# Kernel optimization log

Hardware: AMD Instinct MI355X
Metric: run time of the kernel (lower is better)

Reference implementation:

```python
import jax, jax.numpy as jnp
import numpy as np

C = 1.0
SQC = C ** 0.5
EPS = 1e-15

def _artanh(x):
    return jnp.arctanh(jnp.clip(x, -1 + 1e-5, 1 - 1e-5))

def _norm(x):
    return jnp.sqrt(jnp.maximum(jnp.sum(x * x, -1, keepdims=True), EPS))

def expmap0(u):
    un = _norm(u)
    return jnp.tanh(SQC * un) * u / (SQC * un)

def logmap0(x):
    xn = _norm(x)
    return _artanh(SQC * xn) * x / (SQC * xn)

def project(x):
    maxnorm = (1.0 - 1e-3) / SQC
    xn = _norm(x)
    return jnp.where(xn > maxnorm, x / xn * maxnorm, x)

def mobius_add(x, y):
    x2 = jnp.sum(x * x, -1, keepdims=True)
    y2 = jnp.sum(y * y, -1, keepdims=True)
    xy = jnp.sum(x * y, -1, keepdims=True)
    num = (1 + 2 * C * xy + C * y2) * x + (1 - C * x2) * y
    den = 1 + 2 * C * xy + C * C * x2 * y2
    return num / jnp.maximum(den, EPS)

def mobius_matvec(M, x):
    xn = _norm(x)
    Mx = x @ M.T
    Mxn = _norm(Mx)
    res = jnp.tanh(Mxn / xn * _artanh(SQC * xn)) * Mx / (Mxn * SQC)
    return jnp.where(Mxn <= 1e-7, jnp.zeros_like(res), res)

def mobius_pointwise_mul(w, x):
    xn = _norm(x)
    wx = w * x
    wxn = _norm(wx)
    res = jnp.tanh(wxn / xn * _artanh(SQC * xn)) * wx / (wxn * SQC)
    return jnp.where(wxn <= 1e-7, jnp.zeros_like(res), res)

def mobius_scalar_mul(r, x):
    # r: [B,1] scalars, x: [P] point -> [B,P]
    xn = _norm(x)
    return jnp.tanh(r * _artanh(SQC * xn)) * x / (xn * SQC)

def poincare_dist(x, y):
    return 2.0 / SQC * _artanh(SQC * _norm(mobius_add(-x, y)))

def dist2plane(x, p, a):
    # x: [B,P], p,a: [K,P] -> [B,K]
    diff = mobius_add(-p[None, :, :], x[:, None, :])  # [B,K,P]
    diff2 = jnp.sum(diff * diff, -1)
    sc_da = jnp.sum(diff * a[None, :, :], -1)
    a_norm = jnp.sqrt(jnp.maximum(jnp.sum(a * a, -1), EPS))  # [K]
    num = 2 * SQC * sc_da
    den = jnp.maximum((1 - C * diff2) * a_norm[None, :], EPS)
    return jnp.arcsinh(num / den) / SQC

def one_rnn_transform(W, h, U, x, b):
    Wh = mobius_matvec(W, h)
    Ux = mobius_matvec(U, x)
    return mobius_add(mobius_add(Wh, Ux), b)

def mobius_gru(x_seq, w_ih, w_hh, b, h0):
    # x_seq: [S,B,E]; w_ih: [3,H,E]; w_hh: [3,H,H]; b: [3,H]
    W_ir, W_ih_, W_iz = w_ih[0], w_ih[1], w_ih[2]
    W_hr, W_hh_, W_hz = w_hh[0], w_hh[1], w_hh[2]
    b_r, b_h, b_z = b[0], b[1], b[2]

    def cell(h, x):
        z = jax.nn.sigmoid(logmap0(one_rnn_transform(W_hz, h, W_iz, x, b_z)))
        r = jax.nn.sigmoid(logmap0(one_rnn_transform(W_hr, h, W_ir, x, b_r)))
        rh = mobius_pointwise_mul(r, h)
        h_tilde = one_rnn_transform(W_hh_, rh, W_ih_, x, b_h)
        delta = mobius_add(-h, h_tilde)
        h_new = mobius_add(h, mobius_pointwise_mul(z, delta))
        return h_new, None

    h_final, _ = jax.lax.scan(cell, h0, x_seq)
    return h_final

def mobius_linear(x, W, b):
    return project(mobius_add(mobius_matvec(W, x), b))


def setup_inputs() -> dict:
    key = jax.random.key(0)
    ks = jax.random.split(key, 20)
    V, E, H, P, K, B, S = 32000, 256, 512, 256, 2, 512, 100
    inp = {
        "embedding": jax.random.normal(ks[0], (V, E), jnp.float32) * 0.1,
        "w_ih_src": jax.random.normal(ks[1], (3, H, E), jnp.float32) * 0.05,
        "w_hh_src": jax.random.normal(ks[2], (3, H, H), jnp.float32) * 0.05,
        "b_src": jax.random.normal(ks[3], (3, H), jnp.float32) * 0.01,
        "w_ih_tgt": jax.random.normal(ks[4], (3, H, E), jnp.float32) * 0.05,
        "w_hh_tgt": jax.random.normal(ks[5], (3, H, H), jnp.float32) * 0.05,
        "b_tgt": jax.random.normal(ks[6], (3, H), jnp.float32) * 0.01,
        "wp_src": jax.random.normal(ks[7], (P, H), jnp.float32) * 0.05,
        "bp_src": jax.random.normal(ks[8], (P,), jnp.float32) * 0.01,
        "wp_tgt": jax.random.normal(ks[9], (P, H), jnp.float32) * 0.05,
        "bp_tgt": jax.random.normal(ks[10], (P,), jnp.float32) * 0.01,
        "dist_bias": jax.random.normal(ks[11], (P,), jnp.float32) * 0.01,
        "plane_p": jax.random.normal(ks[12], (K, P), jnp.float32) * 0.01,
        "plane_a": jax.random.normal(ks[13], (K, P), jnp.float32) * 0.1,
        "source_tokens": jax.random.randint(ks[14], (B, S), 0, V, jnp.int32),
        "target_tokens": jax.random.randint(ks[15], (B, S), 0, V, jnp.int32),
        "alignment": jax.random.randint(ks[16], (B,), 0, B, jnp.int32),
    }
    return inp


def reference(embedding, w_ih_src, w_hh_src, b_src, w_ih_tgt, w_hh_tgt, b_tgt,
              wp_src, bp_src, wp_tgt, bp_tgt, dist_bias, plane_p, plane_a,
              source_tokens, target_tokens, alignment):
    B, S = source_tokens.shape
    H = w_hh_src.shape[-1]
    # euclidean embeddings lifted to the Poincare ball (embedding_type='eucl', hyp cell)
    src = expmap0(embedding[source_tokens]).transpose(1, 0, 2)  # [S,B,E]
    tgt = expmap0(embedding[target_tokens]).transpose(1, 0, 2)
    h0 = jnp.zeros((B, H), src.dtype)
    h_src = mobius_gru(src, w_ih_src, w_hh_src, b_src, h0)
    h_tgt = mobius_gru(tgt, w_ih_tgt, w_hh_tgt, b_tgt, h0)
    h_tgt = h_tgt[alignment]
    src_proj = mobius_linear(h_src, wp_src, bp_src)
    tgt_proj = mobius_linear(h_tgt, wp_tgt, bp_tgt)
    projected = mobius_add(src_proj, tgt_proj)
    d2 = poincare_dist(h_src, h_tgt) ** 2  # [B,1]
    bias = mobius_scalar_mul(d2, dist_bias)  # [B,P]
    projected = mobius_add(projected, bias)
    logits = dist2plane(projected, plane_p, plane_a)  # [B,K]
    return logits
```

## Files before the change

kernel.cpp:

```cpp
#include <hip/hip_runtime.h>
#include <hip/hip_bf16.h>

#define EPSF 1e-15f

__device__ __forceinline__ float artanh_c(float x) {
  x = fminf(fmaxf(x, -1.f + 1e-5f), 1.f - 1e-5f);
  return 0.5f * log1pf(2.f * x / (1.f - x));
}
__device__ __forceinline__ float sigmoidf(float x) {
  return 1.f / (1.f + expf(-x));
}

template<int N>
__device__ __forceinline__ void block_reduce(float* v) {
  __shared__ float s[4][N];
  __syncthreads();
  const int lane = threadIdx.x & 63;
  const int wv = threadIdx.x >> 6;
#pragma unroll
  for (int n = 0; n < N; n++) {
    float x = v[n];
#pragma unroll
    for (int o = 32; o > 0; o >>= 1) x += __shfl_down(x, o);
    if (lane == 0) s[wv][n] = x;
  }
  __syncthreads();
#pragma unroll
  for (int n = 0; n < N; n++) v[n] = s[0][n] + s[1][n] + s[2][n] + s[3][n];
}

__global__ __launch_bounds__(256) void k_tok(
    const float* __restrict__ emb, const int* __restrict__ src_t,
    const int* __restrict__ tgt_t, float4* __restrict__ tokf)
{
  const int item = blockIdx.x * 4 + (threadIdx.x >> 6);
  const int lane = threadIdx.x & 63;
  const int g = item / 51200;
  const int rem = item - g * 51200;
  const int b = rem / 100, s = rem - b * 100;
  const int tok = (g ? tgt_t : src_t)[b * 100 + s];
  const float4 v = ((const float4*)(emb + (size_t)tok * 256))[lane];
  float ss = v.x*v.x + v.y*v.y + v.z*v.z + v.w*v.w;
#pragma unroll
  for (int o = 32; o > 0; o >>= 1) ss += __shfl_xor(ss, o);
  if (lane == 0) {
    const float un = sqrtf(fmaxf(ss, EPSF));
    const float fac = tanhf(un) / un;
    const float xn = sqrtf(fmaxf(fac * fac * ss, EPSF));
    const float axn = artanh_c(xn);
    tokf[item] = make_float4(fac, xn, axn, un);
  }
}

__global__ __launch_bounds__(256) void kx0(
    const float* __restrict__ emb, const int* __restrict__ src_t,
    const int* __restrict__ tgt_t, const float4* __restrict__ tokf,
    float* __restrict__ xb)
{
  const int row = blockIdx.x;
  const int t = threadIdx.x;
  const int g = row >> 9, b = row & 511;
  const int tok = (g ? tgt_t : src_t)[b * 100];
  const float fac = tokf[(g * 512 + b) * 100].x;
  xb[(size_t)row * 256 + t] = fac * emb[(size_t)tok * 256 + t];
}

__global__ __launch_bounds__(256) void gemm_k(
    int mode,
    const float* __restrict__ hbuf, const float* __restrict__ xbuf,
    const float* __restrict__ rhbuf,
    const float* __restrict__ w_ih_src, const float* __restrict__ w_hh_src,
    const float* __restrict__ w_ih_tgt, const float* __restrict__ w_hh_tgt,
    const float* __restrict__ wp_src, const float* __restrict__ wp_tgt,
    const int* __restrict__ alignment,
    float* __restrict__ out)
{
  const int rt = blockIdx.x, ct = blockIdx.y;
  const int rowBase = rt * 64;
  const int tid = threadIdx.x;
  int kdim, ldo, colBase;
  const float* W;
  const float* Abase;
  int gather = 0;
  if (mode == 0) {
    const int chunk = ct >> 3;
    colBase = ct * 64; ldo = 2560;
    const int g = rowBase >> 9;
    const float* wih = g ? w_ih_tgt : w_ih_src;
    const float* whh = g ? w_hh_tgt : w_hh_src;
    if (chunk == 0)      { W = whh + 2 * 512 * 512; Abase = hbuf; kdim = 512; }
    else if (chunk == 1) { W = whh;                 Abase = hbuf; kdim = 512; }
    else {
      kdim = 256; Abase = xbuf;
      W = (chunk == 2) ? (wih + 2 * 512 * 256) : ((chunk == 3) ? wih : (wih + 512 * 256));
    }
    W += (size_t)((ct & 7) * 64) * kdim;
  } else if (mode == 1) {
    const int g = rowBase >> 9;
    W = (g ? w_hh_tgt : w_hh_src) + 512 * 512 + (size_t)(ct * 64) * 512;
    Abase = rhbuf; kdim = 512; ldo = 512; colBase = ct * 64;
  } else {
    const int chunk = ct >> 2;
    colBase = ct * 64; ldo = 512; kdim = 512;
    W = (chunk ? wp_tgt : wp_src) + (size_t)((ct & 3) * 64) * 512;
    Abase = hbuf;
    gather = chunk;
  }
  const int ar = tid >> 2, ak = (tid & 3) * 4;
  int arow = rowBase + ar;
  if (mode == 2 && gather) arow = 512 + alignment[arow];
  const float* Arow = Abase + (size_t)arow * kdim;
  const float* Wrow = W + (size_t)(tid >> 2) * kdim + (tid & 3) * 4;

  __shared__ __align__(16) float As[16][68];
  __shared__ __align__(16) float Bs[16][68];
  float acc[4][4] = {{0.f}};
  const int ty = tid >> 4, tx = tid & 15;

  for (int k0 = 0; k0 < kdim; k0 += 16) {
    const float4 av = *(const float4*)(Arow + k0 + ak);
    const float4 bv = *(const float4*)(Wrow + k0);
    const int bj = tid >> 2;
    As[ak + 0][ar] = av.x; As[ak + 1][ar] = av.y; As[ak + 2][ar] = av.z; As[ak + 3][ar] = av.w;
    Bs[ak + 0][bj] = bv.x; Bs[ak + 1][bj] = bv.y; Bs[ak + 2][bj] = bv.z; Bs[ak + 3][bj] = bv.w;
    __syncthreads();
#pragma unroll
    for (int kk = 0; kk < 16; kk++) {
      const float4 a4 = *(const float4*)(&As[kk][ty * 4]);
      const float4 b4 = *(const float4*)(&Bs[kk][tx * 4]);
      acc[0][0] += a4.x * b4.x; acc[0][1] += a4.x * b4.y; acc[0][2] += a4.x * b4.z; acc[0][3] += a4.x * b4.w;
      acc[1][0] += a4.y * b4.x; acc[1][1] += a4.y * b4.y; acc[1][2] += a4.y * b4.z; acc[1][3] += a4.y * b4.w;
      acc[2][0] += a4.z * b4.x; acc[2][1] += a4.z * b4.y; acc[2][2] += a4.z * b4.z; acc[2][3] += a4.z * b4.w;
      acc[3][0] += a4.w * b4.x; acc[3][1] += a4.w * b4.y; acc[3][2] += a4.w * b4.z; acc[3][3] += a4.w * b4.w;
    }
    __syncthreads();
  }
#pragma unroll
  for (int r = 0; r < 4; r++) {
    float4 o; o.x = acc[r][0]; o.y = acc[r][1]; o.z = acc[r][2]; o.w = acc[r][3];
    *(float4*)(out + (size_t)(rowBase + ty * 4 + r) * ldo + colBase + tx * 4) = o;
  }
}

__global__ __launch_bounds__(256) void k2_gates(
    const float* __restrict__ g1, const float* __restrict__ hb,
    const float* __restrict__ b_src, const float* __restrict__ b_tgt,
    const float4* __restrict__ tokf,
    float* __restrict__ zb, float* __restrict__ rhb,
    float* __restrict__ uhxb, float* __restrict__ rn, int s)
{
  const int row = blockIdx.x;
  const int g = row >> 9, b = row & 511;
  const int t = threadIdx.x;
  const float* bb = g ? b_tgt : b_src;
  const float4 tf = tokf[(g * 512 + b) * 100 + s];
  const float xn_x = tf.y, axn_x = tf.z;
  const float* grow = g1 + (size_t)row * 2560;
  const float* hrow = hb + (size_t)row * 512;

  float h[2], whz[2], whr[2], uxz[2], uxr[2], uxh[2], bz[2], br[2];
  float r6[6] = {0, 0, 0, 0, 0, 0};
#pragma unroll
  for (int e = 0; e < 2; e++) {
    const int j = t + e * 256;
    h[e] = hrow[j];
    whz[e] = grow[j];        whr[e] = grow[512 + j];
    uxz[e] = grow[1024 + j]; uxr[e] = grow[1536 + j];
    uxh[e] = grow[2048 + j];
    bz[e] = bb[1024 + j];    br[e] = bb[j];
    r6[0] += h[e] * h[e];     r6[1] += whz[e] * whz[e]; r6[2] += whr[e] * whr[e];
    r6[3] += uxz[e] * uxz[e]; r6[4] += uxr[e] * uxr[e]; r6[5] += uxh[e] * uxh[e];
  }
  block_reduce<6>(r6);
  const float sh2 = r6[0];
  const float xn_h = sqrtf(fmaxf(sh2, EPSF)), axn_h = artanh_c(xn_h);

  const float mz = sqrtf(fmaxf(r6[1], EPSF)); const float tz = tanhf(mz / xn_h * axn_h);
  const float sz = (mz <= 1e-7f) ? 0.f : tz / mz; const float x2z = (mz <= 1e-7f) ? 0.f : tz * tz;
  const float mr = sqrtf(fmaxf(r6[2], EPSF)); const float tr = tanhf(mr / xn_h * axn_h);
  const float sr = (mr <= 1e-7f) ? 0.f : tr / mr; const float x2r = (mr <= 1e-7f) ? 0.f : tr * tr;
  const float muz = sqrtf(fmaxf(r6[3], EPSF)); const float tuz = tanhf(muz / xn_x * axn_x);
  const float suz = (muz <= 1e-7f) ? 0.f : tuz / muz; const float y2z = (muz <= 1e-7f) ? 0.f : tuz * tuz;
  const float mur = sqrtf(fmaxf(r6[4], EPSF)); const float tur = tanhf(mur / xn_x * axn_x);
  const float sur = (mur <= 1e-7f) ? 0.f : tur / mur; const float y2r = (mur <= 1e-7f) ? 0.f : tur * tur;
  const float muh = sqrtf(fmaxf(r6[5], EPSF)); const float tuh = tanhf(muh / xn_x * axn_x);
  const float suh = (muh <= 1e-7f) ? 0.f : tuh / muh; const float y2u = (muh <= 1e-7f) ? 0.f : tuh * tuh;

  float Wz[2], Uz[2], Wr[2], Ur[2];
  float dd[2] = {0, 0};
#pragma unroll
  for (int e = 0; e < 2; e++) {
    Wz[e] = sz * whz[e]; Uz[e] = suz * uxz[e];
    Wr[e] = sr * whr[e]; Ur[e] = sur * uxr[e];
    dd[0] += Wz[e] * Uz[e]; dd[1] += Wr[e] * Ur[e];
  }
  block_reduce<2>(dd);
  float t1z[2], t1r[2];
  {
    const float xy = dd[0];
    const float iv = 1.f / fmaxf(1.f + 2.f * xy + x2z * y2z, EPSF);
    const float c1 = 1.f + 2.f * xy + y2z, c2 = 1.f - x2z;
#pragma unroll
    for (int e = 0; e < 2; e++) t1z[e] = (c1 * Wz[e] + c2 * Uz[e]) * iv;
  }
  {
    const float xy = dd[1];
    const float iv = 1.f / fmaxf(1.f + 2.f * xy + x2r * y2r, EPSF);
    const float c1 = 1.f + 2.f * xy + y2r, c2 = 1.f - x2r;
#pragma unroll
    for (int e = 0; e < 2; e++) t1r[e] = (c1 * Wr[e] + c2 * Ur[e]) * iv;
  }
  float r6b[6] = {0, 0, 0, 0, 0, 0};
#pragma unroll
  for (int e = 0; e < 2; e++) {
    r6b[0] += t1z[e] * t1z[e]; r6b[1] += t1z[e] * bz[e]; r6b[2] += bz[e] * bz[e];
    r6b[3] += t1r[e] * t1r[e]; r6b[4] += t1r[e] * br[e]; r6b[5] += br[e] * br[e];
  }
  block_reduce<6>(r6b);
  float t2z[2], t2r[2];
  {
    const float x2 = r6b[0], xy = r6b[1], y2 = r6b[2];
    const float iv = 1.f / fmaxf(1.f + 2.f * xy + x2 * y2, EPSF);
    const float c1 = 1.f + 2.f * xy + y2, c2 = 1.f - x2;
#pragma unroll
    for (int e = 0; e < 2; e++) t2z[e] = (c1 * t1z[e] + c2 * bz[e]) * iv;
  }
  {
    const float x2 = r6b[3], xy = r6b[4], y2 = r6b[5];
    const float iv = 1.f / fmaxf(1.f + 2.f * xy + x2 * y2, EPSF);
    const float c1 = 1.f + 2.f * xy + y2, c2 = 1.f - x2;
#pragma unroll
    for (int e = 0; e < 2; e++) t2r[e] = (c1 * t1r[e] + c2 * br[e]) * iv;
  }
  float nn[2] = {0, 0};
#pragma unroll
  for (int e = 0; e < 2; e++) { nn[0] += t2z[e] * t2z[e]; nn[1] += t2r[e] * t2r[e]; }
  block_reduce<2>(nn);
  const float nz = sqrtf(fmaxf(nn[0], EPSF)); const float fz = artanh_c(nz) / nz;
  const float nr = sqrtf(fmaxf(nn[1], EPSF)); const float fr = artanh_c(nr) / nr;
  float zz[2], wx[2];
  float rw[1] = {0};
#pragma unroll
  for (int e = 0; e < 2; e++) {
    zz[e] = sigmoidf(fz * t2z[e]);
    const float rr = sigmoidf(fr * t2r[e]);
    wx[e] = rr * h[e];
    rw[0] += wx[e] * wx[e];
  }
  block_reduce<1>(rw);
  const float wxn = sqrtf(fmaxf(rw[0], EPSF));
  const float trh = tanhf(wxn / xn_h * axn_h);
  const float srh = (wxn <= 1e-7f) ? 0.f : trh / wxn;
  const float xn_rh = (wxn <= 1e-7f) ? sqrtf(EPSF) : fmaxf(trh, sqrtf(EPSF));
  const float axn_rh = artanh_c(xn_rh);
#pragma unroll
  for (int e = 0; e < 2; e++) {
    const int j = t + e * 256;
    zb[(size_t)row * 512 + j] = zz[e];
    rhb[(size_t)row * 512 + j] = srh * wx[e];
    uhxb[(size_t)row * 512 + j] = suh * uxh[e];
  }
  if (t == 0) {
    float* r8 = rn + row * 8;
    r8[0] = xn_h; r8[1] = axn_h; r8[2] = xn_rh; r8[3] = axn_rh; r8[4] = y2u; r8[5] = sh2;
  }
}

__global__ __launch_bounds__(256) void k4_update(
    const float* __restrict__ htm, const float* __restrict__ uhxb,
    const float* __restrict__ zb, float* __restrict__ hb,
    const float* __restrict__ b_src, const float* __restrict__ b_tgt,
    const float* __restrict__ rn, const float4* __restrict__ tokf,
    const int* __restrict__ src_t, const int* __restrict__ tgt_t,
    const float* __restrict__ emb, float* __restrict__ xb, int s)
{
  const int row = blockIdx.x;
  const int g = row >> 9, b = row & 511;
  const int t = threadIdx.x;
  const float* bb = g ? b_tgt : b_src;
  const float* r8 = rn + row * 8;
  const float xn_rh = r8[2], axn_rh = r8[3], y2u = r8[4], sh2 = r8[5];

  float mt_[2], ux[2], z[2], h[2], bh[2];
  float rA[2] = {0, 0};
#pragma unroll
  for (int e = 0; e < 2; e++) {
    const int j = t + e * 256;
    mt_[e] = htm[(size_t)row * 512 + j];
    ux[e] = uhxb[(size_t)row * 512 + j];
    z[e] = zb[(size_t)row * 512 + j];
    h[e] = hb[(size_t)row * 512 + j];
    bh[e] = bb[512 + j];
    rA[0] += mt_[e] * mt_[e];
    rA[1] += mt_[e] * ux[e];
  }
  block_reduce<2>(rA);
  const float m = sqrtf(fmaxf(rA[0], EPSF));
  const float tt = tanhf(m / xn_rh * axn_rh);
  const float st = (m <= 1e-7f) ? 0.f : tt / m;
  const float x2 = (m <= 1e-7f) ? 0.f : tt * tt;
  float t1[2];
  {
    const float xy = st * rA[1];
    const float iv = 1.f / fmaxf(1.f + 2.f * xy + x2 * y2u, EPSF);
    const float c1 = 1.f + 2.f * xy + y2u, c2 = 1.f - x2;
#pragma unroll
    for (int e = 0; e < 2; e++) t1[e] = (c1 * (st * mt_[e]) + c2 * ux[e]) * iv;
  }
  float rB[3] = {0, 0, 0};
#pragma unroll
  for (int e = 0; e < 2; e++) {
    rB[0] += t1[e] * t1[e]; rB[1] += t1[e] * bh[e]; rB[2] += bh[e] * bh[e];
  }
  block_reduce<3>(rB);
  float ht[2];
  {
    const float x2b = rB[0], xy = rB[1], y2 = rB[2];
    const float iv = 1.f / fmaxf(1.f + 2.f * xy + x2b * y2, EPSF);
    const float c1 = 1.f + 2.f * xy + y2, c2 = 1.f - x2b;
#pragma unroll
    for (int e = 0; e < 2; e++) ht[e] = (c1 * t1[e] + c2 * bh[e]) * iv;
  }
  float rC[2] = {0, 0};
#pragma unroll
  for (int e = 0; e < 2; e++) { rC[0] += ht[e] * ht[e]; rC[1] += h[e] * ht[e]; }
  block_reduce<2>(rC);
  float delta[2];
  {
    const float y2 = rC[0], xy = -rC[1];
    const float iv = 1.f / fmaxf(1.f + 2.f * xy + sh2 * y2, EPSF);
    const float c1 = 1.f + 2.f * xy + y2, c2 = 1.f - sh2;
#pragma unroll
    for (int e = 0; e < 2; e++) delta[e] = (c1 * (-h[e]) + c2 * ht[e]) * iv;
  }
  float rD[3] = {0, 0, 0};
#pragma unroll
  for (int e = 0; e < 2; e++) {
    const float w = z[e] * delta[e];
    rD[0] += delta[e] * delta[e];
    rD[1] += w * w;
    rD[2] += h[e] * w;
  }
  block_reduce<3>(rD);
  const float dn = sqrtf(fmaxf(rD[0], EPSF));
  const float axnd = artanh_c(dn);
  const float wxn = sqrtf(fmaxf(rD[1], EPSF));
  const float tzd = tanhf(wxn / dn * axnd);
  const float szd = (wxn <= 1e-7f) ? 0.f : tzd / wxn;
  const float y2zd = (wxn <= 1e-7f) ? 0.f : tzd * tzd;
  {
    const float xy = szd * rD[2];
    const float iv = 1.f / fmaxf(1.f + 2.f * xy + sh2 * y2zd, EPSF);
    const float c1 = 1.f + 2.f * xy + y2zd, c2 = 1.f - sh2;
#pragma unroll
    for (int e = 0; e < 2; e++) {
      const int j = t + e * 256;
      hb[(size_t)row * 512 + j] = (c1 * h[e] + c2 * (szd * z[e] * delta[e])) * iv;
    }
  }
  if (s + 1 < 100) {
    const int tok = (g ? tgt_t : src_t)[b * 100 + s + 1];
    const float fac = tokf[(g * 512 + b) * 100 + s + 1].x;
    xb[(size_t)row * 256 + t] = fac * emb[(size_t)tok * 256 + t];
  }
}

__global__ __launch_bounds__(256) void k_head(
    const float* __restrict__ hb, const float* __restrict__ mxb,
    const float* __restrict__ bp_src, const float* __restrict__ bp_tgt,
    const float* __restrict__ dist_bias, const float* __restrict__ plane_p,
    const float* __restrict__ plane_a, const int* __restrict__ alignment,
    float* __restrict__ outp)
{
  const int b = blockIdx.x;
  const int t = threadIdx.x;
  const int arow = 512 + alignment[b];
  float hs[2], htg[2];
  hs[0] = hb[(size_t)b * 512 + t];      hs[1] = hb[(size_t)b * 512 + 256 + t];
  htg[0] = hb[(size_t)arow * 512 + t];  htg[1] = hb[(size_t)arow * 512 + 256 + t];
  const float mxs = mxb[(size_t)b * 512 + t];
  const float mxt = mxb[(size_t)b * 512 + 256 + t];
  const float bps = bp_src[t], bpt = bp_tgt[t], db = dist_bias[t];
  const float pp0 = plane_p[t], pp1 = plane_p[256 + t];
  const float pa0 = plane_a[t], pa1 = plane_a[256 + t];

  float rA[5] = {0, 0, 0, 0, 0};
#pragma unroll
  for (int e = 0; e < 2; e++) {
    rA[0] += hs[e] * hs[e]; rA[1] += htg[e] * htg[e]; rA[2] += hs[e] * htg[e];
  }
  rA[3] = mxs * mxs; rA[4] = mxt * mxt;
  block_reduce<5>(rA);
  const float shs = rA[0], sht = rA[1], dot_st = rA[2];
  const float xns = sqrtf(fmaxf(shs, EPSF)), axns = artanh_c(xns);
  const float xnt = sqrtf(fmaxf(sht, EPSF)), axnt = artanh_c(xnt);
  const float ms = sqrtf(fmaxf(rA[3], EPSF)); const float ts = tanhf(ms / xns * axns);
  const float ss = (ms <= 1e-7f) ? 0.f : ts / ms; const float x2s = (ms <= 1e-7f) ? 0.f : ts * ts;
  const float mt = sqrtf(fmaxf(rA[4], EPSF)); const float tt = tanhf(mt / xnt * axnt);
  const float st = (mt <= 1e-7f) ? 0.f : tt / mt; const float x2t = (mt <= 1e-7f) ? 0.f : tt * tt;
  const float vs = ss * mxs, vt = st * mxt;

  float rB[5] = {bps * bps, vs * bps, bpt * bpt, vt * bpt, db * db};
  block_reduce<5>(rB);
  float ps, pt;
  {
    const float y2 = rB[0], xy = rB[1];
    const float iv = 1.f / fmaxf(1.f + 2.f * xy + x2s * y2, EPSF);
    ps = ((1.f + 2.f * xy + y2) * vs + (1.f - x2s) * bps) * iv;
  }
  {
    const float y2 = rB[2], xy = rB[3];
    const float iv = 1.f / fmaxf(1.f + 2.f * xy + x2t * y2, EPSF);
    pt = ((1.f + 2.f * xy + y2) * vt + (1.f - x2t) * bpt) * iv;
  }
  float rC[2] = {ps * ps, pt * pt};
  block_reduce<2>(rC);
  {
    const float n = sqrtf(fmaxf(rC[0], EPSF));
    if (n > 0.999f) ps *= 0.999f / n;
  }
  {
    const float n = sqrtf(fmaxf(rC[1], EPSF));
    if (n > 0.999f) pt *= 0.999f / n;
  }
  float df[2];
  {
    const float xy = -dot_st;
    const float iv = 1.f / fmaxf(1.f + 2.f * xy + shs * sht, EPSF);
    const float c1 = 1.f + 2.f * xy + sht, c2 = 1.f - shs;
#pragma unroll
    for (int e = 0; e < 2; e++) df[e] = (c1 * (-hs[e]) + c2 * htg[e]) * iv;
  }
  float rD[4] = {ps * ps, pt * pt, ps * pt, df[0] * df[0] + df[1] * df[1]};
  block_reduce<4>(rD);
  float pr;
  {
    const float x2 = rD[0], y2 = rD[1], xy = rD[2];
    const float iv = 1.f / fmaxf(1.f + 2.f * xy + x2 * y2, EPSF);
    pr = ((1.f + 2.f * xy + y2) * ps + (1.f - x2) * pt) * iv;
  }
  const float dn = sqrtf(fmaxf(rD[3], EPSF));
  const float dist = 2.f * artanh_c(dn);
  const float d2v = dist * dist;
  const float dbn = sqrtf(fmaxf(rB[4], EPSF));
  const float biasv = tanhf(d2v * artanh_c(dbn)) * db / dbn;

  float rE[3] = {pr * pr, biasv * biasv, pr * biasv};
  block_reduce<3>(rE);
  float pr2;
  {
    const float x2 = rE[0], y2 = rE[1], xy = rE[2];
    const float iv = 1.f / fmaxf(1.f + 2.f * xy + x2 * y2, EPSF);
    pr2 = ((1.f + 2.f * xy + y2) * pr + (1.f - x2) * biasv) * iv;
  }
  float rF[5] = {pp0 * pp0, pp0 * pr2, pp1 * pp1, pp1 * pr2, pr2 * pr2};
  block_reduce<5>(rF);
  float d0, d1;
  {
    const float x2 = rF[0], xy = -rF[1], y2 = rF[4];
    const float iv = 1.f / fmaxf(1.f + 2.f * xy + x2 * y2, EPSF);
    d0 = ((1.f + 2.f * xy + y2) * (-pp0) + (1.f - x2) * pr2) * iv;
  }
  {
    const float x2 = rF[2], xy = -rF[3], y2 = rF[4];
    const float iv = 1.f / fmaxf(1.f + 2.f * xy + x2 * y2, EPSF);
    d1 = ((1.f + 2.f * xy + y2) * (-pp1) + (1.f - x2) * pr2) * iv;
  }
  float rG[6] = {d0 * d0, d0 * pa0, pa0 * pa0, d1 * d1, d1 * pa1, pa1 * pa1};
  block_reduce<6>(rG);
  if (t == 0) {
    const float an0 = sqrtf(fmaxf(rG[2], EPSF));
    const float an1 = sqrtf(fmaxf(rG[5], EPSF));
    const float l0 = asinhf(2.f * rG[1] / fmaxf((1.f - rG[0]) * an0, EPSF));
    const float l1 = asinhf(2.f * rG[4] / fmaxf((1.f - rG[3]) * an1, EPSF));
    outp[b * 2 + 0] = l0;
    outp[b * 2 + 1] = l1;
  }
}

extern "C" void kernel_launch(void* const* d_in, const int* in_sizes, int n_in,
                              void* d_out, int out_size, void* d_ws, size_t ws_size,
                              hipStream_t stream) {
  const float* emb       = (const float*)d_in[0];
  const float* w_ih_src  = (const float*)d_in[1];
  const float* w_hh_src  = (const float*)d_in[2];
  const float* b_src     = (const float*)d_in[3];
  const float* w_ih_tgt  = (const float*)d_in[4];
  const float* w_hh_tgt  = (const float*)d_in[5];
  const float* b_tgt     = (const float*)d_in[6];
  const float* wp_src    = (const float*)d_in[7];
  const float* bp_src    = (const float*)d_in[8];
  const float* wp_tgt    = (const float*)d_in[9];
  const float* bp_tgt    = (const float*)d_in[10];
  const float* dist_bias = (const float*)d_in[11];
  const float* plane_p   = (const float*)d_in[12];
  const float* plane_a   = (const float*)d_in[13];
  const int* src_t       = (const int*)d_in[14];
  const int* tgt_t       = (const int*)d_in[15];
  const int* alignment   = (const int*)d_in[16];
  float* outp            = (float*)d_out;

  float* ws = (float*)d_ws;
  float* hbuf = ws + 0;
  float* xbuf = ws + 524288;
  float* g1   = ws + 786432;
  float* zb   = ws + 3407872;
  float* rhb  = ws + 3932160;
  float* uhxb = ws + 4456448;
  float* htm  = ws + 4980736;
  float* rn   = ws + 5505024;
  float4* tokf = (float4*)(ws + 5513216);
  float* mxb  = ws + 5922816;

  hipMemsetAsync(hbuf, 0, 1024 * 512 * sizeof(float), stream);
  k_tok<<<25600, 256, 0, stream>>>(emb, src_t, tgt_t, tokf);
  kx0<<<1024, 256, 0, stream>>>(emb, src_t, tgt_t, tokf, xbuf);
  for (int s = 0; s < 100; s++) {
    gemm_k<<<dim3(16, 40), 256, 0, stream>>>(0, hbuf, xbuf, rhb,
        w_ih_src, w_hh_src, w_ih_tgt, w_hh_tgt, wp_src, wp_tgt, alignment, g1);
    k2_gates<<<1024, 256, 0, stream>>>(g1, hbuf, b_src, b_tgt, tokf, zb, rhb, uhxb, rn, s);
    gemm_k<<<dim3(16, 8), 256, 0, stream>>>(1, hbuf, xbuf, rhb,
        w_ih_src, w_hh_src, w_ih_tgt, w_hh_tgt, wp_src, wp_tgt, alignment, htm);
    k4_update<<<1024, 256, 0, stream>>>(htm, uhxb, zb, hbuf, b_src, b_tgt, rn, tokf,
        src_t, tgt_t, emb, xbuf, s);
  }
  gemm_k<<<dim3(8, 8), 256, 0, stream>>>(2, hbuf, xbuf, rhb,
      w_ih_src, w_hh_src, w_ih_tgt, w_hh_tgt, wp_src, wp_tgt, alignment, mxb);
  k_head<<<512, 256, 0, stream>>>(hbuf, mxb, bp_src, bp_tgt, dist_bias,
      plane_p, plane_a, alignment, outp);
}
```

Baseline: 8.037 ms.

## Fuse the recurrent GRU loop into one persistent MFMA kernel with split-bf16 weights

The per-timestep launch sequence (two GEMMs plus gate and update kernels, 400 launches) is replaced by one persistent kernel. Each of 64 blocks owns 16 batch rows of one sequence and runs all 100 steps internally. The GEMMs use bf16 MFMA with hi/lo split operands (three products) to approximate fp32 accuracy. Weights are pre-swizzled into an MFMA-friendly layout by a conversion kernel, and token embedding and expmap are computed inline. The aim is to remove launch overhead and global round-trips, at the cost of using only 64 blocks, which may underuse the GPU and push weight reads through L2 every step.

```diff
diff --git a/kernel.cpp b/kernel.cpp
--- a/kernel.cpp
+++ b/kernel.cpp
@@ -2,75 +2,464 @@
 #include <hip/hip_bf16.h>
 
 #define EPSF 1e-15f
+
+typedef __hip_bfloat16 bf16;
+typedef __attribute__((ext_vector_type(8))) short short8;
+typedef __attribute__((ext_vector_type(4))) float f32x4;
+
+#define F4E(v,i) ((i)==0?(v).x:((i)==1?(v).y:((i)==2?(v).z:(v).w)))
+#define U4E(v,i) ((i)==0?(v).x:((i)==1?(v).y:((i)==2?(v).z:(v).w)))
 
 __device__ __forceinline__ float artanh_c(float x) {
   x = fminf(fmaxf(x, -1.f + 1e-5f), 1.f - 1e-5f);
   return 0.5f * log1pf(2.f * x / (1.f - x));
 }
-__device__ __forceinline__ float sigmoidf(float x) {
-  return 1.f / (1.f + expf(-x));
-}
-
-template<int N>
-__device__ __forceinline__ void block_reduce(float* v) {
-  __shared__ float s[4][N];
-  __syncthreads();
-  const int lane = threadIdx.x & 63;
-  const int wv = threadIdx.x >> 6;
-#pragma unroll
-  for (int n = 0; n < N; n++) {
-    float x = v[n];
-#pragma unroll
-    for (int o = 32; o > 0; o >>= 1) x += __shfl_down(x, o);
-    if (lane == 0) s[wv][n] = x;
-  }
-  __syncthreads();
-#pragma unroll
-  for (int n = 0; n < N; n++) v[n] = s[0][n] + s[1][n] + s[2][n] + s[3][n];
-}
-
-__global__ __launch_bounds__(256) void k_tok(
-    const float* __restrict__ emb, const int* __restrict__ src_t,
-    const int* __restrict__ tgt_t, float4* __restrict__ tokf)
-{
-  const int item = blockIdx.x * 4 + (threadIdx.x >> 6);
-  const int lane = threadIdx.x & 63;
-  const int g = item / 51200;
-  const int rem = item - g * 51200;
-  const int b = rem / 100, s = rem - b * 100;
-  const int tok = (g ? tgt_t : src_t)[b * 100 + s];
-  const float4 v = ((const float4*)(emb + (size_t)tok * 256))[lane];
-  float ss = v.x*v.x + v.y*v.y + v.z*v.z + v.w*v.w;
-#pragma unroll
-  for (int o = 32; o > 0; o >>= 1) ss += __shfl_xor(ss, o);
-  if (lane == 0) {
-    const float un = sqrtf(fmaxf(ss, EPSF));
-    const float fac = tanhf(un) / un;
-    const float xn = sqrtf(fmaxf(fac * fac * ss, EPSF));
-    const float axn = artanh_c(xn);
-    tokf[item] = make_float4(fac, xn, axn, un);
-  }
-}
-
-__global__ __launch_bounds__(256) void kx0(
-    const float* __restrict__ emb, const int* __restrict__ src_t,
-    const int* __restrict__ tgt_t, const float4* __restrict__ tokf,
-    float* __restrict__ xb)
-{
-  const int row = blockIdx.x;
-  const int t = threadIdx.x;
-  const int g = row >> 9, b = row & 511;
-  const int tok = (g ? tgt_t : src_t)[b * 100];
-  const float fac = tokf[(g * 512 + b) * 100].x;
-  xb[(size_t)row * 256 + t] = fac * emb[(size_t)tok * 256 + t];
-}
-
-__global__ __launch_bounds__(256) void gemm_k(
-    int mode,
-    const float* __restrict__ hbuf, const float* __restrict__ xbuf,
-    const float* __restrict__ rhbuf,
+__device__ __forceinline__ float sigmoidf(float x) { return 1.f / (1.f + expf(-x)); }
+__device__ __forceinline__ float wave_sum(float x) {
+#pragma unroll
+  for (int o = 32; o > 0; o >>= 1) x += __shfl_xor(x, o);
+  return x;
+}
+__device__ __forceinline__ float bu2f(ushort u) { return __uint_as_float(((unsigned)u) << 16); }
+__device__ __forceinline__ ushort f2bu(float v) {
+  bf16 t = __float2bfloat16(v);
+  union { bf16 b; ushort u; } c; c.b = t; return c.u;
+}
+__device__ __forceinline__ void split2(float v, ushort& h, ushort& l) {
+  h = f2bu(v); l = f2bu(v - bu2f(h));
+}
+
+__global__ __launch_bounds__(256) void k_wconv(
     const float* __restrict__ w_ih_src, const float* __restrict__ w_hh_src,
     const float* __restrict__ w_ih_tgt, const float* __restrict__ w_hh_tgt,
+    bf16* __restrict__ W0h, bf16* __restrict__ W0l,
+    bf16* __restrict__ W1h, bf16* __restrict__ W1l)
+{
+  const int idx = blockIdx.x * 256 + threadIdx.x;
+  float v;
+  if (idx < 1835008) {
+    const int g = idx / 917504, p = idx % 917504;
+    const float* wih = g ? w_ih_tgt : w_ih_src;
+    const float* whh = g ? w_hh_tgt : w_hh_src;
+    if (p < 524288) {
+      const int unit = p >> 9, r = p & 511, lane = r >> 3, e = r & 7;
+      const int ct = unit >> 4, ki = unit & 15;
+      const int col = ct*16 + (lane & 15), k = ki*32 + (lane >> 4)*8 + e;
+      v = (col < 512) ? whh[524288 + col*512 + k]
+                      : whh[(col - 512)*512 + k];
+    } else {
+      const int q = p - 524288;
+      const int unit = q >> 9, r = q & 511, lane = r >> 3, e = r & 7;
+      const int ct = unit >> 3, ki = unit & 7;
+      const int col = ct*16 + (lane & 15), k = ki*32 + (lane >> 4)*8 + e;
+      v = (col < 512)  ? wih[262144 + col*256 + k]
+        : (col < 1024) ? wih[(col - 512)*256 + k]
+                       : wih[131072 + (col - 1024)*256 + k];
+    }
+    ushort hh, ll; split2(v, hh, ll);
+    ((ushort*)W0h)[idx] = hh; ((ushort*)W0l)[idx] = ll;
+  } else {
+    const int j = idx - 1835008;
+    if (j >= 524288) return;
+    const int g = j >> 18, p = j & 262143;
+    const float* whh = g ? w_hh_tgt : w_hh_src;
+    const int unit = p >> 9, r = p & 511, lane = r >> 3, e = r & 7;
+    const int ct = unit >> 4, ki = unit & 15;
+    const int col = ct*16 + (lane & 15), k = ki*32 + (lane >> 4)*8 + e;
+    v = whh[262144 + col*512 + k];
+    ushort hh, ll; split2(v, hh, ll);
+    ((ushort*)W1h)[j] = hh; ((ushort*)W1l)[j] = ll;
+  }
+}
+
+__device__ __forceinline__ void gate_row(
+    const float h[8], const float whz[8], const float whr[8],
+    const float uxz[8], const float uxr[8], const float uxh[8],
+    const float bz[8], const float br[8],
+    float xn_x, float axn_x,
+    float rh[8], float pz[8], float puhx[8],
+    float& o_xnrh, float& o_axnrh, float& o_y2u, float& o_sh2)
+{
+  float r60=0, r61=0, r62=0, r63=0, r64_=0, r65=0;
+#pragma unroll
+  for (int e = 0; e < 8; e++) {
+    r60 += h[e]*h[e];     r61 += whz[e]*whz[e]; r62 += whr[e]*whr[e];
+    r63 += uxz[e]*uxz[e]; r64_ += uxr[e]*uxr[e]; r65 += uxh[e]*uxh[e];
+  }
+  r60 = wave_sum(r60); r61 = wave_sum(r61); r62 = wave_sum(r62);
+  r63 = wave_sum(r63); r64_ = wave_sum(r64_); r65 = wave_sum(r65);
+  const float sh2 = r60;
+  const float xn_h = sqrtf(fmaxf(sh2, EPSF)), axn_h = artanh_c(xn_h);
+  const float mz = sqrtf(fmaxf(r61, EPSF)); const float tz = tanhf(mz / xn_h * axn_h);
+  const float sz = (mz <= 1e-7f) ? 0.f : tz/mz; const float x2z = (mz <= 1e-7f) ? 0.f : tz*tz;
+  const float mr = sqrtf(fmaxf(r62, EPSF)); const float tr_ = tanhf(mr / xn_h * axn_h);
+  const float sr = (mr <= 1e-7f) ? 0.f : tr_/mr; const float x2r = (mr <= 1e-7f) ? 0.f : tr_*tr_;
+  const float muz = sqrtf(fmaxf(r63, EPSF)); const float tuz = tanhf(muz / xn_x * axn_x);
+  const float suz = (muz <= 1e-7f) ? 0.f : tuz/muz; const float y2z = (muz <= 1e-7f) ? 0.f : tuz*tuz;
+  const float mur = sqrtf(fmaxf(r64_, EPSF)); const float tur = tanhf(mur / xn_x * axn_x);
+  const float sur = (mur <= 1e-7f) ? 0.f : tur/mur; const float y2r = (mur <= 1e-7f) ? 0.f : tur*tur;
+  const float muh = sqrtf(fmaxf(r65, EPSF)); const float tuh = tanhf(muh / xn_x * axn_x);
+  const float suh = (muh <= 1e-7f) ? 0.f : tuh/muh; const float y2u = (muh <= 1e-7f) ? 0.f : tuh*tuh;
+
+  float dd0 = 0, dd1 = 0;
+#pragma unroll
+  for (int e = 0; e < 8; e++) {
+    dd0 += (sz*whz[e])*(suz*uxz[e]);
+    dd1 += (sr*whr[e])*(sur*uxr[e]);
+  }
+  dd0 = wave_sum(dd0); dd1 = wave_sum(dd1);
+  float t1z[8], t1r[8];
+  {
+    const float iv = 1.f / fmaxf(1.f + 2.f*dd0 + x2z*y2z, EPSF);
+    const float c1 = 1.f + 2.f*dd0 + y2z, c2 = 1.f - x2z;
+#pragma unroll
+    for (int e = 0; e < 8; e++) t1z[e] = (c1*(sz*whz[e]) + c2*(suz*uxz[e])) * iv;
+  }
+  {
+    const float iv = 1.f / fmaxf(1.f + 2.f*dd1 + x2r*y2r, EPSF);
+    const float c1 = 1.f + 2.f*dd1 + y2r, c2 = 1.f - x2r;
+#pragma unroll
+    for (int e = 0; e < 8; e++) t1r[e] = (c1*(sr*whr[e]) + c2*(sur*uxr[e])) * iv;
+  }
+  float e0=0, e1=0, e2=0, e3=0, e4=0, e5=0;
+#pragma unroll
+  for (int e = 0; e < 8; e++) {
+    e0 += t1z[e]*t1z[e]; e1 += t1z[e]*bz[e]; e2 += bz[e]*bz[e];
+    e3 += t1r[e]*t1r[e]; e4 += t1r[e]*br[e]; e5 += br[e]*br[e];
+  }
+  e0 = wave_sum(e0); e1 = wave_sum(e1); e2 = wave_sum(e2);
+  e3 = wave_sum(e3); e4 = wave_sum(e4); e5 = wave_sum(e5);
+  float t2z[8], t2r[8];
+  {
+    const float iv = 1.f / fmaxf(1.f + 2.f*e1 + e0*e2, EPSF);
+    const float c1 = 1.f + 2.f*e1 + e2, c2 = 1.f - e0;
+#pragma unroll
+    for (int e = 0; e < 8; e++) t2z[e] = (c1*t1z[e] + c2*bz[e]) * iv;
+  }
+  {
+    const float iv = 1.f / fmaxf(1.f + 2.f*e4 + e3*e5, EPSF);
+    const float c1 = 1.f + 2.f*e4 + e5, c2 = 1.f - e3;
+#pragma unroll
+    for (int e = 0; e < 8; e++) t2r[e] = (c1*t1r[e] + c2*br[e]) * iv;
+  }
+  float n0 = 0, n1 = 0;
+#pragma unroll
+  for (int e = 0; e < 8; e++) { n0 += t2z[e]*t2z[e]; n1 += t2r[e]*t2r[e]; }
+  n0 = wave_sum(n0); n1 = wave_sum(n1);
+  const float nz = sqrtf(fmaxf(n0, EPSF)); const float fz = artanh_c(nz) / nz;
+  const float nr = sqrtf(fmaxf(n1, EPSF)); const float frg = artanh_c(nr) / nr;
+  float wx[8];
+  float rw = 0;
+#pragma unroll
+  for (int e = 0; e < 8; e++) {
+    pz[e] = sigmoidf(fz * t2z[e]);
+    const float rr = sigmoidf(frg * t2r[e]);
+    wx[e] = rr * h[e];
+    rw += wx[e]*wx[e];
+  }
+  rw = wave_sum(rw);
+  const float wxn = sqrtf(fmaxf(rw, EPSF));
+  const float trh = tanhf(wxn / xn_h * axn_h);
+  const float srh = (wxn <= 1e-7f) ? 0.f : trh / wxn;
+  const float xn_rh = (wxn <= 1e-7f) ? sqrtf(EPSF) : fmaxf(trh, sqrtf(EPSF));
+#pragma unroll
+  for (int e = 0; e < 8; e++) { rh[e] = srh * wx[e]; puhx[e] = suh * uxh[e]; }
+  o_xnrh = xn_rh; o_axnrh = artanh_c(xn_rh); o_y2u = y2u; o_sh2 = sh2;
+}
+
+__device__ __forceinline__ void update_row(
+    const float mt_[8], const float bh[8],
+    const float pz[8], const float puhx[8], const float phv[8],
+    float p_xnrh, float p_axnrh, float p_y2u, float p_sh2,
+    float hnew[8])
+{
+  float a0s = 0, a1s = 0;
+#pragma unroll
+  for (int e = 0; e < 8; e++) { a0s += mt_[e]*mt_[e]; a1s += mt_[e]*puhx[e]; }
+  a0s = wave_sum(a0s); a1s = wave_sum(a1s);
+  const float m = sqrtf(fmaxf(a0s, EPSF));
+  const float tt = tanhf(m / p_xnrh * p_axnrh);
+  const float st = (m <= 1e-7f) ? 0.f : tt/m;
+  const float x2 = (m <= 1e-7f) ? 0.f : tt*tt;
+  float t1[8];
+  {
+    const float xy = st * a1s;
+    const float iv = 1.f / fmaxf(1.f + 2.f*xy + x2*p_y2u, EPSF);
+    const float c1 = 1.f + 2.f*xy + p_y2u, c2 = 1.f - x2;
+#pragma unroll
+    for (int e = 0; e < 8; e++) t1[e] = (c1*(st*mt_[e]) + c2*puhx[e]) * iv;
+  }
+  float b0s = 0, b1s = 0, b2s = 0;
+#pragma unroll
+  for (int e = 0; e < 8; e++) { b0s += t1[e]*t1[e]; b1s += t1[e]*bh[e]; b2s += bh[e]*bh[e]; }
+  b0s = wave_sum(b0s); b1s = wave_sum(b1s); b2s = wave_sum(b2s);
+  float ht[8];
+  {
+    const float iv = 1.f / fmaxf(1.f + 2.f*b1s + b0s*b2s, EPSF);
+    const float c1 = 1.f + 2.f*b1s + b2s, c2 = 1.f - b0s;
+#pragma unroll
+    for (int e = 0; e < 8; e++) ht[e] = (c1*t1[e] + c2*bh[e]) * iv;
+  }
+  float c0s = 0, c1s = 0;
+#pragma unroll
+  for (int e = 0; e < 8; e++) { c0s += ht[e]*ht[e]; c1s += phv[e]*ht[e]; }
+  c0s = wave_sum(c0s); c1s = wave_sum(c1s);
+  float delta[8];
+  {
+    const float xy = -c1s;
+    const float iv = 1.f / fmaxf(1.f + 2.f*xy + p_sh2*c0s, EPSF);
+    const float c1 = 1.f + 2.f*xy + c0s, c2 = 1.f - p_sh2;
+#pragma unroll
+    for (int e = 0; e < 8; e++) delta[e] = (c1*(-phv[e]) + c2*ht[e]) * iv;
+  }
+  float d0s = 0, d1s = 0, d2s = 0;
+#pragma unroll
+  for (int e = 0; e < 8; e++) {
+    const float ww = pz[e]*delta[e];
+    d0s += delta[e]*delta[e]; d1s += ww*ww; d2s += phv[e]*ww;
+  }
+  d0s = wave_sum(d0s); d1s = wave_sum(d1s); d2s = wave_sum(d2s);
+  const float dn = sqrtf(fmaxf(d0s, EPSF));
+  const float axnd = artanh_c(dn);
+  const float wxn = sqrtf(fmaxf(d1s, EPSF));
+  const float tzd = tanhf(wxn / dn * axnd);
+  const float szd = (wxn <= 1e-7f) ? 0.f : tzd/wxn;
+  const float y2zd = (wxn <= 1e-7f) ? 0.f : tzd*tzd;
+  const float xy = szd * d2s;
+  const float iv = 1.f / fmaxf(1.f + 2.f*xy + p_sh2*y2zd, EPSF);
+  const float c1 = 1.f + 2.f*xy + y2zd, c2 = 1.f - p_sh2;
+#pragma unroll
+  for (int e = 0; e < 8; e++) hnew[e] = (c1*phv[e] + c2*(szd*pz[e]*delta[e])) * iv;
+}
+
+__global__ __launch_bounds__(512) void k_rnn(
+    const float* __restrict__ emb, const int* __restrict__ src_t,
+    const int* __restrict__ tgt_t, const float* __restrict__ b_src,
+    const float* __restrict__ b_tgt,
+    const bf16* __restrict__ W0h_, const bf16* __restrict__ W0l_,
+    const bf16* __restrict__ W1h_, const bf16* __restrict__ W1l_,
+    float* __restrict__ yws, float* __restrict__ htmws,
+    float* __restrict__ hbuf)
+{
+  const int bid = blockIdx.x, tid = threadIdx.x;
+  const int w = tid >> 6, lane = tid & 63;
+  const int fr = lane & 15, kg = lane >> 4;
+  const int g = bid & 1, b16 = bid >> 1;
+  const bf16* W0h = W0h_ + (size_t)g * 917504;
+  const bf16* W0l = W0l_ + (size_t)g * 917504;
+  const bf16* W1h = W1h_ + (size_t)g * 262144;
+  const bf16* W1l = W1l_ + (size_t)g * 262144;
+  const int* toks = g ? tgt_t : src_t;
+  const float* bb = g ? b_tgt : b_src;
+  float* ysl = yws + (size_t)bid * 40960;
+  float* hsl = htmws + (size_t)bid * 8192;
+
+  __shared__ char L[65536];
+  for (int i = tid; i < 2048; i += 512) ((float4*)L)[i] = make_float4(0.f,0.f,0.f,0.f);
+
+  float p_xnx[2], p_axnx[2];
+  float pz_[2][8], puhx_[2][8], phh_[2][8];
+  float p_xnrh[2], p_axnrh[2], p_y2u[2], p_sh2[2];
+
+#define XLOAD(RI, TOKIDX)                                                        \
+  {                                                                              \
+    const int row = w*2 + (RI);                                                  \
+    const int tok = toks[(b16*16 + row)*100 + (TOKIDX)];                         \
+    const float4 ev = ((const float4*)(emb + (size_t)tok * 256))[lane];          \
+    float ss = ev.x*ev.x + ev.y*ev.y + ev.z*ev.z + ev.w*ev.w;                    \
+    ss = wave_sum(ss);                                                           \
+    const float un = sqrtf(fmaxf(ss, EPSF));                                     \
+    const float fac = tanhf(un) / un;                                            \
+    const float xnv = sqrtf(fmaxf(fac*fac*ss, EPSF));                            \
+    p_xnx[RI] = xnv; p_axnx[RI] = artanh_c(xnv);                                 \
+    ushort th[4], tl[4];                                                         \
+    split2(fac*ev.x, th[0], tl[0]); split2(fac*ev.y, th[1], tl[1]);              \
+    split2(fac*ev.z, th[2], tl[2]); split2(fac*ev.w, th[3], tl[3]);              \
+    const unsigned xo = (unsigned)((row*512 + lane*8) ^ ((row & 7) << 4));       \
+    *(ushort4*)(L + 32768 + xo) = make_ushort4(th[0],th[1],th[2],th[3]);         \
+    *(ushort4*)(L + 40960 + xo) = make_ushort4(tl[0],tl[1],tl[2],tl[3]);         \
+  }
+
+  XLOAD(0, 0)
+  XLOAD(1, 0)
+  __syncthreads();
+
+  for (int s = 0; s < 100; s++) {
+    {
+      const f32x4 z4 = {0.f,0.f,0.f,0.f};
+      f32x4 acc[8];
+#pragma unroll
+      for (int t = 0; t < 8; t++) acc[t] = z4;
+      for (int ki = 0; ki < 16; ki++) {
+        const unsigned ao = (unsigned)((fr*1024 + ki*64 + kg*16) ^ ((fr & 7) << 4));
+        const short8 aHi = *(const short8*)(L + ao);
+        const short8 aLo = *(const short8*)(L + 16384 + ao);
+#pragma unroll
+        for (int t = 0; t < 8; t++) {
+          const size_t u = (size_t)(((w*8 + t)*16 + ki)*512) + lane*8;
+          const short8 bHi = *(const short8*)(W0h + u);
+          const short8 bLo = *(const short8*)(W0l + u);
+          acc[t] = __builtin_amdgcn_mfma_f32_16x16x32_bf16(aHi, bHi, acc[t], 0,0,0);
+          acc[t] = __builtin_amdgcn_mfma_f32_16x16x32_bf16(aHi, bLo, acc[t], 0,0,0);
+          acc[t] = __builtin_amdgcn_mfma_f32_16x16x32_bf16(aLo, bHi, acc[t], 0,0,0);
+        }
+      }
+#pragma unroll
+      for (int t = 0; t < 8; t++) {
+        const int colb = (w*8 + t)*16 + fr;
+#pragma unroll
+        for (int r = 0; r < 4; r++)
+          ysl[(size_t)(kg*4 + r)*2560 + colb] = acc[t][r];
+      }
+    }
+    {
+      const f32x4 z4 = {0.f,0.f,0.f,0.f};
+      f32x4 acc[12];
+#pragma unroll
+      for (int t = 0; t < 12; t++) acc[t] = z4;
+      for (int ki = 0; ki < 8; ki++) {
+        const unsigned ao = (unsigned)((fr*512 + ki*64 + kg*16) ^ ((fr & 7) << 4));
+        const short8 aHi = *(const short8*)(L + 32768 + ao);
+        const short8 aLo = *(const short8*)(L + 40960 + ao);
+#pragma unroll
+        for (int t = 0; t < 12; t++) {
+          const size_t u = 524288 + (size_t)(((w*12 + t)*8 + ki)*512) + lane*8;
+          const short8 bHi = *(const short8*)(W0h + u);
+          const short8 bLo = *(const short8*)(W0l + u);
+          acc[t] = __builtin_amdgcn_mfma_f32_16x16x32_bf16(aHi, bHi, acc[t], 0,0,0);
+          acc[t] = __builtin_amdgcn_mfma_f32_16x16x32_bf16(aHi, bLo, acc[t], 0,0,0);
+          acc[t] = __builtin_amdgcn_mfma_f32_16x16x32_bf16(aLo, bHi, acc[t], 0,0,0);
+        }
+      }
+#pragma unroll
+      for (int t = 0; t < 12; t++) {
+        const int colb = 1024 + (w*12 + t)*16 + fr;
+#pragma unroll
+        for (int r = 0; r < 4; r++)
+          ysl[(size_t)(kg*4 + r)*2560 + colb] = acc[t][r];
+      }
+    }
+    __syncthreads();
+
+#define PH2_ROW(RI)                                                              \
+    {                                                                            \
+      const int row = w*2 + (RI);                                                \
+      const float* grow = ysl + row * 2560;                                      \
+      float h[8], whz[8], whr[8], uxz[8], uxr[8], uxh[8], bz[8], br[8];          \
+      _Pragma("unroll")                                                          \
+      for (int q = 0; q < 2; q++) {                                              \
+        const int j4 = lane + 64*q;                                              \
+        const unsigned ho = (unsigned)((row*1024 + j4*8) ^ ((row & 7) << 4));    \
+        const ushort4 hh4 = *(const ushort4*)(L + ho);                           \
+        const ushort4 hl4 = *(const ushort4*)(L + 16384 + ho);                   \
+        const float4 vz  = ((const float4*)grow)[j4];                            \
+        const float4 vr  = ((const float4*)(grow + 512))[j4];                    \
+        const float4 uz  = ((const float4*)(grow + 1024))[j4];                   \
+        const float4 ur  = ((const float4*)(grow + 1536))[j4];                   \
+        const float4 uh  = ((const float4*)(grow + 2048))[j4];                   \
+        const float4 vbz = ((const float4*)(bb + 1024))[j4];                     \
+        const float4 vbr = ((const float4*)bb)[j4];                              \
+        _Pragma("unroll")                                                        \
+        for (int i = 0; i < 4; i++) {                                            \
+          const int e = q*4 + i;                                                 \
+          h[e] = bu2f(U4E(hh4,i)) + bu2f(U4E(hl4,i));                            \
+          whz[e] = F4E(vz,i); whr[e] = F4E(vr,i);                                \
+          uxz[e] = F4E(uz,i); uxr[e] = F4E(ur,i); uxh[e] = F4E(uh,i);            \
+          bz[e] = F4E(vbz,i); br[e] = F4E(vbr,i);                               \
+        }                                                                        \
+      }                                                                          \
+      float rh[8];                                                               \
+      gate_row(h, whz, whr, uxz, uxr, uxh, bz, br, p_xnx[RI], p_axnx[RI],        \
+               rh, pz_[RI], puhx_[RI],                                           \
+               p_xnrh[RI], p_axnrh[RI], p_y2u[RI], p_sh2[RI]);                   \
+      _Pragma("unroll")                                                          \
+      for (int e = 0; e < 8; e++) phh_[RI][e] = h[e];                            \
+      _Pragma("unroll")                                                          \
+      for (int q = 0; q < 2; q++) {                                              \
+        const int j4 = lane + 64*q;                                              \
+        const unsigned ro = (unsigned)((row*1024 + j4*8) ^ ((row & 7) << 4));    \
+        ushort th[4], tl[4];                                                     \
+        _Pragma("unroll")                                                        \
+        for (int i = 0; i < 4; i++) split2(rh[q*4+i], th[i], tl[i]);             \
+        *(ushort4*)(L + 32768 + ro) = make_ushort4(th[0],th[1],th[2],th[3]);     \
+        *(ushort4*)(L + 49152 + ro) = make_ushort4(tl[0],tl[1],tl[2],tl[3]);     \
+      }                                                                          \
+    }
+
+    PH2_ROW(0)
+    PH2_ROW(1)
+    __syncthreads();
+
+    {
+      const f32x4 z4 = {0.f,0.f,0.f,0.f};
+      f32x4 acc[4];
+#pragma unroll
+      for (int t = 0; t < 4; t++) acc[t] = z4;
+      for (int ki = 0; ki < 16; ki++) {
+        const unsigned ao = (unsigned)((fr*1024 + ki*64 + kg*16) ^ ((fr & 7) << 4));
+        const short8 aHi = *(const short8*)(L + 32768 + ao);
+        const short8 aLo = *(const short8*)(L + 49152 + ao);
+#pragma unroll
+        for (int t = 0; t < 4; t++) {
+          const size_t u = (size_t)(((w*4 + t)*16 + ki)*512) + lane*8;
+          const short8 bHi = *(const short8*)(W1h + u);
+          const short8 bLo = *(const short8*)(W1l + u);
+          acc[t] = __builtin_amdgcn_mfma_f32_16x16x32_bf16(aHi, bHi, acc[t], 0,0,0);
+          acc[t] = __builtin_amdgcn_mfma_f32_16x16x32_bf16(aHi, bLo, acc[t], 0,0,0);
+          acc[t] = __builtin_amdgcn_mfma_f32_16x16x32_bf16(aLo, bHi, acc[t], 0,0,0);
+        }
+      }
+#pragma unroll
+      for (int t = 0; t < 4; t++) {
+        const int colb = (w*4 + t)*16 + fr;
+#pragma unroll
+        for (int r = 0; r < 4; r++)
+          hsl[(size_t)(kg*4 + r)*512 + colb] = acc[t][r];
+      }
+    }
+    __syncthreads();
+
+#define PH4_ROW(RI)                                                              \
+    {                                                                            \
+      const int row = w*2 + (RI);                                                \
+      float mt_[8], bh[8];                                                       \
+      _Pragma("unroll")                                                          \
+      for (int q = 0; q < 2; q++) {                                              \
+        const int j4 = lane + 64*q;                                              \
+        const float4 vm = ((const float4*)(hsl + row*512))[j4];                  \
+        const float4 vb = ((const float4*)(bb + 512))[j4];                       \
+        _Pragma("unroll")                                                        \
+        for (int i = 0; i < 4; i++) {                                            \
+          mt_[q*4+i] = F4E(vm,i); bh[q*4+i] = F4E(vb,i);                         \
+        }                                                                        \
+      }                                                                          \
+      float hnew[8];                                                             \
+      update_row(mt_, bh, pz_[RI], puhx_[RI], phh_[RI],                          \
+                 p_xnrh[RI], p_axnrh[RI], p_y2u[RI], p_sh2[RI], hnew);           \
+      _Pragma("unroll")                                                          \
+      for (int q = 0; q < 2; q++) {                                              \
+        const int j4 = lane + 64*q;                                              \
+        const unsigned ho = (unsigned)((row*1024 + j4*8) ^ ((row & 7) << 4));    \
+        ushort th[4], tl[4];                                                     \
+        _Pragma("unroll")                                                        \
+        for (int i = 0; i < 4; i++) split2(hnew[q*4+i], th[i], tl[i]);           \
+        *(ushort4*)(L + ho) = make_ushort4(th[0],th[1],th[2],th[3]);             \
+        *(ushort4*)(L + 16384 + ho) = make_ushort4(tl[0],tl[1],tl[2],tl[3]);     \
+        if (s == 99)                                                             \
+          ((float4*)(hbuf + (size_t)(g*512 + b16*16 + row)*512))[j4] =           \
+              make_float4(hnew[q*4], hnew[q*4+1], hnew[q*4+2], hnew[q*4+3]);     \
+      }                                                                          \
+      if (s + 1 < 100) XLOAD(RI, s + 1)                                          \
+    }
+
+    PH4_ROW(0)
+    PH4_ROW(1)
+    __syncthreads();
+  }
+}
+
+__global__ __launch_bounds__(256) void gemm_k(
+    const float* __restrict__ hbuf,
     const float* __restrict__ wp_src, const float* __restrict__ wp_tgt,
     const int* __restrict__ alignment,
     float* __restrict__ out)
@@ -78,38 +467,13 @@
   const int rt = blockIdx.x, ct = blockIdx.y;
   const int rowBase = rt * 64;
   const int tid = threadIdx.x;
-  int kdim, ldo, colBase;
-  const float* W;
-  const float* Abase;
-  int gather = 0;
-  if (mode == 0) {
-    const int chunk = ct >> 3;
-    colBase = ct * 64; ldo = 2560;
-    const int g = rowBase >> 9;
-    const float* wih = g ? w_ih_tgt : w_ih_src;
-    const float* whh = g ? w_hh_tgt : w_hh_src;
-    if (chunk == 0)      { W = whh + 2 * 512 * 512; Abase = hbuf; kdim = 512; }
-    else if (chunk == 1) { W = whh;                 Abase = hbuf; kdim = 512; }
-    else {
-      kdim = 256; Abase = xbuf;
-      W = (chunk == 2) ? (wih + 2 * 512 * 256) : ((chunk == 3) ? wih : (wih + 512 * 256));
-    }
-    W += (size_t)((ct & 7) * 64) * kdim;
-  } else if (mode == 1) {
-    const int g = rowBase >> 9;
-    W = (g ? w_hh_tgt : w_hh_src) + 512 * 512 + (size_t)(ct * 64) * 512;
-    Abase = rhbuf; kdim = 512; ldo = 512; colBase = ct * 64;
-  } else {
-    const int chunk = ct >> 2;
-    colBase = ct * 64; ldo = 512; kdim = 512;
-    W = (chunk ? wp_tgt : wp_src) + (size_t)((ct & 3) * 64) * 512;
-    Abase = hbuf;
-    gather = chunk;
-  }
+  const int chunk = ct >> 2;
+  const int colBase = ct * 64, ldo = 512, kdim = 512;
+  const float* W = (chunk ? wp_tgt : wp_src) + (size_t)((ct & 3) * 64) * 512;
   const int ar = tid >> 2, ak = (tid & 3) * 4;
   int arow = rowBase + ar;
-  if (mode == 2 && gather) arow = 512 + alignment[arow];
-  const float* Arow = Abase + (size_t)arow * kdim;
+  if (chunk) arow = 512 + alignment[arow];
+  const float* Arow = hbuf + (size_t)arow * kdim;
   const float* Wrow = W + (size_t)(tid >> 2) * kdim + (tid & 3) * 4;
 
   __shared__ __align__(16) float As[16][68];
@@ -142,227 +506,22 @@
   }
 }
 
-__global__ __launch_bounds__(256) void k2_gates(
-    const float* __restrict__ g1, const float* __restrict__ hb,
-    const float* __restrict__ b_src, const float* __restrict__ b_tgt,
-    const float4* __restrict__ tokf,
-    float* __restrict__ zb, float* __restrict__ rhb,
-    float* __restrict__ uhxb, float* __restrict__ rn, int s)
-{
-  const int row = blockIdx.x;
-  const int g = row >> 9, b = row & 511;
-  const int t = threadIdx.x;
-  const float* bb = g ? b_tgt : b_src;
-  const float4 tf = tokf[(g * 512 + b) * 100 + s];
-  const float xn_x = tf.y, axn_x = tf.z;
-  const float* grow = g1 + (size_t)row * 2560;
-  const float* hrow = hb + (size_t)row * 512;
-
-  float h[2], whz[2], whr[2], uxz[2], uxr[2], uxh[2], bz[2], br[2];
-  float r6[6] = {0, 0, 0, 0, 0, 0};
-#pragma unroll
-  for (int e = 0; e < 2; e++) {
-    const int j = t + e * 256;
-    h[e] = hrow[j];
-    whz[e] = grow[j];        whr[e] = grow[512 + j];
-    uxz[e] = grow[1024 + j]; uxr[e] = grow[1536 + j];
-    uxh[e] = grow[2048 + j];
-    bz[e] = bb[1024 + j];    br[e] = bb[j];
-    r6[0] += h[e] * h[e];     r6[1] += whz[e] * whz[e]; r6[2] += whr[e] * whr[e];
-    r6[3] += uxz[e] * uxz[e]; r6[4] += uxr[e] * uxr[e]; r6[5] += uxh[e] * uxh[e];
-  }
-  block_reduce<6>(r6);
-  const float sh2 = r6[0];
-  const float xn_h = sqrtf(fmaxf(sh2, EPSF)), axn_h = artanh_c(xn_h);
-
-  const float mz = sqrtf(fmaxf(r6[1], EPSF)); const float tz = tanhf(mz / xn_h * axn_h);
-  const float sz = (mz <= 1e-7f) ? 0.f : tz / mz; const float x2z = (mz <= 1e-7f) ? 0.f : tz * tz;
-  const float mr = sqrtf(fmaxf(r6[2], EPSF)); const float tr = tanhf(mr / xn_h * axn_h);
-  const float sr = (mr <= 1e-7f) ? 0.f : tr / mr; const float x2r = (mr <= 1e-7f) ? 0.f : tr * tr;
-  const float muz = sqrtf(fmaxf(r6[3], EPSF)); const float tuz = tanhf(muz / xn_x * axn_x);
-  const float suz = (muz <= 1e-7f) ? 0.f : tuz / muz; const float y2z = (muz <= 1e-7f) ? 0.f : tuz * tuz;
-  const float mur = sqrtf(fmaxf(r6[4], EPSF)); const float tur = tanhf(mur / xn_x * axn_x);
-  const float sur = (mur <= 1e-7f) ? 0.f : tur / mur; const float y2r = (mur <= 1e-7f) ? 0.f : tur * tur;
-  const float muh = sqrtf(fmaxf(r6[5], EPSF)); const float tuh = tanhf(muh / xn_x * axn_x);
-  const float suh = (muh <= 1e-7f) ? 0.f : tuh / muh; const float y2u = (muh <= 1e-7f) ? 0.f : tuh * tuh;
-
-  float Wz[2], Uz[2], Wr[2], Ur[2];
-  float dd[2] = {0, 0};
-#pragma unroll
-  for (int e = 0; e < 2; e++) {
-    Wz[e] = sz * whz[e]; Uz[e] = suz * uxz[e];
-    Wr[e] = sr * whr[e]; Ur[e] = sur * uxr[e];
-    dd[0] += Wz[e] * Uz[e]; dd[1] += Wr[e] * Ur[e];
-  }
-  block_reduce<2>(dd);
-  float t1z[2], t1r[2];
-  {
-    const float xy = dd[0];
-    const float iv = 1.f / fmaxf(1.f + 2.f * xy + x2z * y2z, EPSF);
-    const float c1 = 1.f + 2.f * xy + y2z, c2 = 1.f - x2z;
-#pragma unroll
-    for (int e = 0; e < 2; e++) t1z[e] = (c1 * Wz[e] + c2 * Uz[e]) * iv;
-  }
-  {
-    const float xy = dd[1];
-    const float iv = 1.f / fmaxf(1.f + 2.f * xy + x2r * y2r, EPSF);
-    const float c1 = 1.f + 2.f * xy + y2r, c2 = 1.f - x2r;
-#pragma unroll
-    for (int e = 0; e < 2; e++) t1r[e] = (c1 * Wr[e] + c2 * Ur[e]) * iv;
-  }
-  float r6b[6] = {0, 0, 0, 0, 0, 0};
-#pragma unroll
-  for (int e = 0; e < 2; e++) {
-    r6b[0] += t1z[e] * t1z[e]; r6b[1] += t1z[e] * bz[e]; r6b[2] += bz[e] * bz[e];
-    r6b[3] += t1r[e] * t1r[e]; r6b[4] += t1r[e] * br[e]; r6b[5] += br[e] * br[e];
-  }
-  block_reduce<6>(r6b);
-  float t2z[2], t2r[2];
-  {
-    const float x2 = r6b[0], xy = r6b[1], y2 = r6b[2];
-    const float iv = 1.f / fmaxf(1.f + 2.f * xy + x2 * y2, EPSF);
-    const float c1 = 1.f + 2.f * xy + y2, c2 = 1.f - x2;
-#pragma unroll
-    for (int e = 0; e < 2; e++) t2z[e] = (c1 * t1z[e] + c2 * bz[e]) * iv;
-  }
-  {
-    const float x2 = r6b[3], xy = r6b[4], y2 = r6b[5];
-    const float iv = 1.f / fmaxf(1.f + 2.f * xy + x2 * y2, EPSF);
-    const float c1 = 1.f + 2.f * xy + y2, c2 = 1.f - x2;
-#pragma unroll
-    for (int e = 0; e < 2; e++) t2r[e] = (c1 * t1r[e] + c2 * br[e]) * iv;
-  }
-  float nn[2] = {0, 0};
-#pragma unroll
-  for (int e = 0; e < 2; e++) { nn[0] += t2z[e] * t2z[e]; nn[1] += t2r[e] * t2r[e]; }
-  block_reduce<2>(nn);
-  const float nz = sqrtf(fmaxf(nn[0], EPSF)); const float fz = artanh_c(nz) / nz;
-  const float nr = sqrtf(fmaxf(nn[1], EPSF)); const float fr = artanh_c(nr) / nr;
-  float zz[2], wx[2];
-  float rw[1] = {0};
-#pragma unroll
-  for (int e = 0; e < 2; e++) {
-    zz[e] = sigmoidf(fz * t2z[e]);
-    const float rr = sigmoidf(fr * t2r[e]);
-    wx[e] = rr * h[e];
-    rw[0] += wx[e] * wx[e];
-  }
-  block_reduce<1>(rw);
-  const float wxn = sqrtf(fmaxf(rw[0], EPSF));
-  const float trh = tanhf(wxn / xn_h * axn_h);
-  const float srh = (wxn <= 1e-7f) ? 0.f : trh / wxn;
-  const float xn_rh = (wxn <= 1e-7f) ? sqrtf(EPSF) : fmaxf(trh, sqrtf(EPSF));
-  const float axn_rh = artanh_c(xn_rh);
-#pragma unroll
-  for (int e = 0; e < 2; e++) {
-    const int j = t + e * 256;
-    zb[(size_t)row * 512 + j] = zz[e];
-    rhb[(size_t)row * 512 + j] = srh * wx[e];
-    uhxb[(size_t)row * 512 + j] = suh * uxh[e];
-  }
-  if (t == 0) {
-    float* r8 = rn + row * 8;
-    r8[0] = xn_h; r8[1] = axn_h; r8[2] = xn_rh; r8[3] = axn_rh; r8[4] = y2u; r8[5] = sh2;
-  }
-}
-
-__global__ __launch_bounds__(256) void k4_update(
-    const float* __restrict__ htm, const float* __restrict__ uhxb,
-    const float* __restrict__ zb, float* __restrict__ hb,
-    const float* __restrict__ b_src, const float* __restrict__ b_tgt,
-    const float* __restrict__ rn, const float4* __restrict__ tokf,
-    const int* __restrict__ src_t, const int* __restrict__ tgt_t,
-    const float* __restrict__ emb, float* __restrict__ xb, int s)
-{
-  const int row = blockIdx.x;
-  const int g = row >> 9, b = row & 511;
-  const int t = threadIdx.x;
-  const float* bb = g ? b_tgt : b_src;
-  const float* r8 = rn + row * 8;
-  const float xn_rh = r8[2], axn_rh = r8[3], y2u = r8[4], sh2 = r8[5];
-
-  float mt_[2], ux[2], z[2], h[2], bh[2];
-  float rA[2] = {0, 0};
-#pragma unroll
-  for (int e = 0; e < 2; e++) {
-    const int j = t + e * 256;
-    mt_[e] = htm[(size_t)row * 512 + j];
-    ux[e] = uhxb[(size_t)row * 512 + j];
-    z[e] = zb[(size_t)row * 512 + j];
-    h[e] = hb[(size_t)row * 512 + j];
-    bh[e] = bb[512 + j];
-    rA[0] += mt_[e] * mt_[e];
-    rA[1] += mt_[e] * ux[e];
-  }
-  block_reduce<2>(rA);
-  const float m = sqrtf(fmaxf(rA[0], EPSF));
-  const float tt = tanhf(m / xn_rh * axn_rh);
-  const float st = (m <= 1e-7f) ? 0.f : tt / m;
-  const float x2 = (m <= 1e-7f) ? 0.f : tt * tt;
-  float t1[2];
-  {
-    const float xy = st * rA[1];
-    const float iv = 1.f / fmaxf(1.f + 2.f * xy + x2 * y2u, EPSF);
-    const float c1 = 1.f + 2.f * xy + y2u, c2 = 1.f - x2;
-#pragma unroll
-    for (int e = 0; e < 2; e++) t1[e] = (c1 * (st * mt_[e]) + c2 * ux[e]) * iv;
-  }
-  float rB[3] = {0, 0, 0};
-#pragma unroll
-  for (int e = 0; e < 2; e++) {
-    rB[0] += t1[e] * t1[e]; rB[1] += t1[e] * bh[e]; rB[2] += bh[e] * bh[e];
-  }
-  block_reduce<3>(rB);
-  float ht[2];
-  {
-    const float x2b = rB[0], xy = rB[1], y2 = rB[2];
-    const float iv = 1.f / fmaxf(1.f + 2.f * xy + x2b * y2, EPSF);
-    const float c1 = 1.f + 2.f * xy + y2, c2 = 1.f - x2b;
-#pragma unroll
-    for (int e = 0; e < 2; e++) ht[e] = (c1 * t1[e] + c2 * bh[e]) * iv;
-  }
-  float rC[2] = {0, 0};
-#pragma unroll
-  for (int e = 0; e < 2; e++) { rC[0] += ht[e] * ht[e]; rC[1] += h[e] * ht[e]; }
-  block_reduce<2>(rC);
-  float delta[2];
-  {
-    const float y2 = rC[0], xy = -rC[1];
-    const float iv = 1.f / fmaxf(1.f + 2.f * xy + sh2 * y2, EPSF);
-    const float c1 = 1.f + 2.f * xy + y2, c2 = 1.f - sh2;
-#pragma unroll
-    for (int e = 0; e < 2; e++) delta[e] = (c1 * (-h[e]) + c2 * ht[e]) * iv;
-  }
-  float rD[3] = {0, 0, 0};
-#pragma unroll
-  for (int e = 0; e < 2; e++) {
-    const float w = z[e] * delta[e];
-    rD[0] += delta[e] * delta[e];
-    rD[1] += w * w;
-    rD[2] += h[e] * w;
-  }
-  block_reduce<3>(rD);
-  const float dn = sqrtf(fmaxf(rD[0], EPSF));
-  const float axnd = artanh_c(dn);
-  const float wxn = sqrtf(fmaxf(rD[1], EPSF));
-  const float tzd = tanhf(wxn / dn * axnd);
-  const float szd = (wxn <= 1e-7f) ? 0.f : tzd / wxn;
-  const float y2zd = (wxn <= 1e-7f) ? 0.f : tzd * tzd;
-  {
-    const float xy = szd * rD[2];
-    const float iv = 1.f / fmaxf(1.f + 2.f * xy + sh2 * y2zd, EPSF);
-    const float c1 = 1.f + 2.f * xy + y2zd, c2 = 1.f - sh2;
-#pragma unroll
-    for (int e = 0; e < 2; e++) {
-      const int j = t + e * 256;
-      hb[(size_t)row * 512 + j] = (c1 * h[e] + c2 * (szd * z[e] * delta[e])) * iv;
-    }
-  }
-  if (s + 1 < 100) {
-    const int tok = (g ? tgt_t : src_t)[b * 100 + s + 1];
-    const float fac = tokf[(g * 512 + b) * 100 + s + 1].x;
-    xb[(size_t)row * 256 + t] = fac * emb[(size_t)tok * 256 + t];
-  }
+template<int N>
+__device__ __forceinline__ void block_reduce(float* v) {
+  __shared__ float s[4][N];
+  __syncthreads();
+  const int lane = threadIdx.x & 63;
+  const int wv = threadIdx.x >> 6;
+#pragma unroll
+  for (int n = 0; n < N; n++) {
+    float x = v[n];
+#pragma unroll
+    for (int o = 32; o > 0; o >>= 1) x += __shfl_down(x, o);
+    if (lane == 0) s[wv][n] = x;
+  }
+  __syncthreads();
+#pragma unroll
+  for (int n = 0; n < N; n++) v[n] = s[0][n] + s[1][n] + s[2][n] + s[3][n];
 }
 
 __global__ __launch_bounds__(256) void k_head(
@@ -471,10 +630,8 @@
   if (t == 0) {
     const float an0 = sqrtf(fmaxf(rG[2], EPSF));
     const float an1 = sqrtf(fmaxf(rG[5], EPSF));
-    const float l0 = asinhf(2.f * rG[1] / fmaxf((1.f - rG[0]) * an0, EPSF));
-    const float l1 = asinhf(2.f * rG[4] / fmaxf((1.f - rG[3]) * an1, EPSF));
-    outp[b * 2 + 0] = l0;
-    outp[b * 2 + 1] = l1;
+    outp[b * 2 + 0] = asinhf(2.f * rG[1] / fmaxf((1.f - rG[0]) * an0, EPSF));
+    outp[b * 2 + 1] = asinhf(2.f * rG[4] / fmaxf((1.f - rG[3]) * an1, EPSF));
   }
 }
 
@@ -500,32 +657,21 @@
   const int* alignment   = (const int*)d_in[16];
   float* outp            = (float*)d_out;
 
-  float* ws = (float*)d_ws;
-  float* hbuf = ws + 0;
-  float* xbuf = ws + 524288;
-  float* g1   = ws + 786432;
-  float* zb   = ws + 3407872;
-  float* rhb  = ws + 3932160;
-  float* uhxb = ws + 4456448;
-  float* htm  = ws + 4980736;
-  float* rn   = ws + 5505024;
-  float4* tokf = (float4*)(ws + 5513216);
-  float* mxb  = ws + 5922816;
-
-  hipMemsetAsync(hbuf, 0, 1024 * 512 * sizeof(float), stream);
-  k_tok<<<25600, 256, 0, stream>>>(emb, src_t, tgt_t, tokf);
-  kx0<<<1024, 256, 0, stream>>>(emb, src_t, tgt_t, tokf, xbuf);
-  for (int s = 0; s < 100; s++) {
-    gemm_k<<<dim3(16, 40), 256, 0, stream>>>(0, hbuf, xbuf, rhb,
-        w_ih_src, w_hh_src, w_ih_tgt, w_hh_tgt, wp_src, wp_tgt, alignment, g1);
-    k2_gates<<<1024, 256, 0, stream>>>(g1, hbuf, b_src, b_tgt, tokf, zb, rhb, uhxb, rn, s);
-    gemm_k<<<dim3(16, 8), 256, 0, stream>>>(1, hbuf, xbuf, rhb,
-        w_ih_src, w_hh_src, w_ih_tgt, w_hh_tgt, wp_src, wp_tgt, alignment, htm);
-    k4_update<<<1024, 256, 0, stream>>>(htm, uhxb, zb, hbuf, b_src, b_tgt, rn, tokf,
-        src_t, tgt_t, emb, xbuf, s);
-  }
-  gemm_k<<<dim3(8, 8), 256, 0, stream>>>(2, hbuf, xbuf, rhb,
-      w_ih_src, w_hh_src, w_ih_tgt, w_hh_tgt, wp_src, wp_tgt, alignment, mxb);
+  char* wsb = (char*)d_ws;
+  float* yws   = (float*)(wsb + 0);
+  float* htmws = (float*)(wsb + 10485760);
+  float* hbuf  = (float*)(wsb + 12582912);
+  float* mxb   = (float*)(wsb + 14680064);
+  bf16*  W0h   = (bf16*)(wsb + 15728640);
+  bf16*  W0l   = (bf16*)(wsb + 19398656);
+  bf16*  W1h   = (bf16*)(wsb + 23068672);
+  bf16*  W1l   = (bf16*)(wsb + 24117248);
+
+  k_wconv<<<9216, 256, 0, stream>>>(w_ih_src, w_hh_src, w_ih_tgt, w_hh_tgt,
+                                    W0h, W0l, W1h, W1l);
+  k_rnn<<<64, 512, 0, stream>>>(emb, src_t, tgt_t, b_src, b_tgt,
+                                W0h, W0l, W1h, W1l, yws, htmws, hbuf);
+  gemm_k<<<dim3(8, 8), 256, 0, stream>>>(hbuf, wp_src, wp_tgt, alignment, mxb);
   k_head<<<512, 256, 0, stream>>>(hbuf, mxb, bp_src, bp_tgt, dist_bias,
-      plane_p, plane_a, alignment, outp);
-}
+                                  plane_p, plane_a, alignment, outp);
+}
```

After: 15.69 ms. 95.2% more time.
